# Optimization experiments

Hardware: AMD Instinct MI355X
Metric: run time of the kernel (lower is better)

The kernel has to match this reference:

```python
import jax, jax.numpy as jnp
import numpy as np

N = 100000
E = 3200000
IN_F = 256
OUT_F = 256
CLAMP = 10.0


def setup_inputs() -> dict:
    key = jax.random.key(0)
    k1, k2, k3, k4, k5 = jax.random.split(key, 5)
    x = jax.random.normal(k1, (N, IN_F), dtype=jnp.float32)
    adj_rows = jnp.sort(jax.random.randint(k2, (E,), 0, N, dtype=jnp.int32))
    adj_cols = jax.random.randint(k3, (E,), 0, N, dtype=jnp.int32)
    adj_vals = jax.random.uniform(k4, (E,), dtype=jnp.float32)
    # glorot-ish init (scaled by 0.1 as in the module)
    stdv = 0.1 * np.sqrt(6.0 / (IN_F + OUT_F))
    weight = jax.random.uniform(k5, (IN_F, OUT_F), dtype=jnp.float32,
                                minval=-stdv, maxval=stdv)
    bias = jnp.zeros((OUT_F,), dtype=jnp.float32)
    return {"x": x, "adj_rows": adj_rows, "adj_cols": adj_cols,
            "adj_vals": adj_vals, "weight": weight, "bias": bias}


def reference(x, adj_rows, adj_cols, adj_vals, weight, bias):
    # clamp input
    x = jnp.clip(x, -CLAMP, CLAMP)
    # dense projection: [N, in] @ [in, out]
    support = jnp.clip(x @ weight, -CLAMP, CLAMP)
    # sparse adjacency SpMM: out[r] += val * support[c] for each edge (r, c)
    msgs = adj_vals[:, None] * support[adj_cols]          # [E, out]
    output = jax.ops.segment_sum(msgs, adj_rows, num_segments=N)
    output = jnp.clip(output, -CLAMP, CLAMP)
    output = output + bias
    output = jax.nn.relu(output)
    return jnp.clip(output, -CLAMP, CLAMP)
```

## Files before the change

kernel.cpp:

```cpp
#include <hip/hip_runtime.h>

#define N_NODES 100000
#define N_EDGES 3200000
#define IN_F    256
#define OUT_F   256
#define CLAMP_V 10.0f

typedef __attribute__((ext_vector_type(8))) short bf16x8;
typedef __attribute__((ext_vector_type(4))) float f32x4;

__device__ __forceinline__ float clampf(float v) {
    return fminf(fmaxf(v, -CLAMP_V), CLAMP_V);
}
__device__ __forceinline__ unsigned f2bf(float f) {
    unsigned u = __float_as_uint(f);
    u += 0x7fffu + ((u >> 16) & 1u);
    return u >> 16;
}
__device__ __forceinline__ unsigned cvt_pk_bf16(float lo, float hi) {
    unsigned r;
    asm("v_cvt_pk_bf16_f32 %0, %1, %2" : "=v"(r) : "v"(lo), "v"(hi));
    return r;
}
__device__ __forceinline__ float bflo(unsigned w) { return __uint_as_float(w << 16); }
__device__ __forceinline__ float bfhi(unsigned w) { return __uint_as_float(w & 0xffff0000u); }

__global__ __launch_bounds__(256) void convert_w(
    const float* __restrict__ w, unsigned short* __restrict__ wt) {
    int i = blockIdx.x * 256 + threadIdx.x;
    int k = i & 255, n = i >> 8;
    float v = w[(size_t)k * OUT_F + n];
    int dst = n * 256 + (((k >> 3) ^ (n & 7)) << 3) + (k & 7);
    wt[dst] = (unsigned short)f2bf(v);
}

__global__ __launch_bounds__(256) void build_row_ptr(
    const int* __restrict__ rows, int* __restrict__ row_ptr) {
    int r = blockIdx.x * blockDim.x + threadIdx.x;
    if (r > N_NODES) return;
    int lo = 0, hi = N_EDGES;
    while (lo < hi) {
        int mid = (lo + hi) >> 1;
        if (rows[mid] < r) lo = mid + 1; else hi = mid;
    }
    row_ptr[r] = lo;
}

__global__ __launch_bounds__(1024) void gemm_mfma(
    const float* __restrict__ x, const unsigned short* __restrict__ wt,
    unsigned* __restrict__ sup8, float* __restrict__ scales) {
    __shared__ uint4 wlds[8192];

    const int t    = threadIdx.x;
    const int lane = t & 63;
    const int w    = t >> 6;
    const int wr   = w >> 2;
    const int wc   = w & 3;
    const int l15  = lane & 15;
    const int l4   = lane >> 4;
    const int blockRow = blockIdx.x * 256;

    {
        const uint4* g = (const uint4*)wt;
        #pragma unroll
        for (int i = 0; i < 8; ++i)
            wlds[i * 1024 + t] = g[i * 1024 + t];
    }

    const float* aptr[4];
    #pragma unroll
    for (int m = 0; m < 4; ++m) {
        int r = blockRow + wr * 64 + m * 16 + l15;
        aptr[m] = x + (size_t)(r < N_NODES ? r : N_NODES - 1) * IN_F + l4 * 8;
    }

    f32x4 acc[4][4];
    #pragma unroll
    for (int m = 0; m < 4; ++m)
        #pragma unroll
        for (int n = 0; n < 4; ++n)
            acc[m][n] = (f32x4)0.f;

    __syncthreads();

    #pragma unroll
    for (int s = 0; s < 8; ++s) {
        bf16x8 a[4], b[4];
        #pragma unroll
        for (int m = 0; m < 4; ++m) {
            float4 u0 = *(const float4*)(aptr[m] + s * 32);
            float4 u1 = *(const float4*)(aptr[m] + s * 32 + 4);
            union { unsigned u[4]; bf16x8 v; } pk;
            pk.u[0] = cvt_pk_bf16(clampf(u0.x), clampf(u0.y));
            pk.u[1] = cvt_pk_bf16(clampf(u0.z), clampf(u0.w));
            pk.u[2] = cvt_pk_bf16(clampf(u1.x), clampf(u1.y));
            pk.u[3] = cvt_pk_bf16(clampf(u1.z), clampf(u1.w));
            a[m] = pk.v;
        }
        #pragma unroll
        for (int n = 0; n < 4; ++n) {
            int ncol  = wc * 64 + n * 16 + l15;
            int chunk = ncol * 32 + ((s * 4 + l4) ^ (ncol & 7));
            b[n] = *(const bf16x8*)&wlds[chunk];
        }
        #pragma unroll
        for (int m = 0; m < 4; ++m)
            #pragma unroll
            for (int n = 0; n < 4; ++n)
                acc[m][n] = __builtin_amdgcn_mfma_f32_16x16x32_bf16(
                    a[m], b[n], acc[m][n], 0, 0, 0);
    }

    __syncthreads();
    {
        char* sl = (char*)wlds;
        #pragma unroll
        for (int m = 0; m < 4; ++m) {
            #pragma unroll
            for (int n = 0; n < 4; ++n) {
                int col2 = (wc * 64 + n * 16 + l15) * 2;
                #pragma unroll
                for (int r = 0; r < 4; ++r) {
                    int row = wr * 64 + m * 16 + l4 * 4 + r;
                    int off = row * 512 + (col2 ^ (((row >> 2) & 3) << 4));
                    *(unsigned short*)(sl + off) = (unsigned short)f2bf(clampf(acc[m][n][r]));
                }
            }
        }
    }
    __syncthreads();

    {
        const uint4* sl4 = (const uint4*)wlds;
        const int row = t >> 2;
        const int qt  = t & 3;
        const int swz = (row >> 2) & 3;

        uint4 c[8];
        float mx = 0.f;
        #pragma unroll
        for (int j = 0; j < 8; ++j) {
            c[j] = sl4[row * 32 + ((qt * 8 + j) ^ swz)];
            const unsigned* cu = (const unsigned*)&c[j];
            #pragma unroll
            for (int q = 0; q < 4; ++q)
                mx = fmaxf(mx, fmaxf(fabsf(bflo(cu[q])), fabsf(bfhi(cu[q]))));
        }
        mx = fmaxf(mx, __shfl_xor(mx, 1));
        mx = fmaxf(mx, __shfl_xor(mx, 2));

        const float inv = 127.f / fmaxf(mx, 1e-30f);
        const int grow = blockRow + row;
        if (grow < N_NODES) {
            unsigned p[16];
            #pragma unroll
            for (int j = 0; j < 8; ++j) {
                const unsigned* cu = (const unsigned*)&c[j];
                #pragma unroll
                for (int q = 0; q < 2; ++q) {
                    unsigned b0 = (unsigned)(int)rintf(bflo(cu[q*2+0]) * inv) + 128u;
                    unsigned b1 = (unsigned)(int)rintf(bfhi(cu[q*2+0]) * inv) + 128u;
                    unsigned b2 = (unsigned)(int)rintf(bflo(cu[q*2+1]) * inv) + 128u;
                    unsigned b3 = (unsigned)(int)rintf(bfhi(cu[q*2+1]) * inv) + 128u;
                    p[j*2+q] = b0 | (b1 << 8) | (b2 << 16) | (b3 << 24);
                }
            }
            uint4* dst = (uint4*)(sup8 + (size_t)grow * 64 + qt * 16);
            #pragma unroll
            for (int j = 0; j < 4; ++j)
                dst[j] = *(const uint4*)&p[j * 4];
            if (qt == 0) scales[grow] = mx * (1.f / 127.f);
        }
    }
}

#define FMAQ(g, vs)                                                       \
    S += (vs);                                                            \
    acc[0] += (vs) * (float)((g).x & 0xffu);                              \
    acc[1] += (vs) * (float)(((g).x >> 8) & 0xffu);                       \
    acc[2] += (vs) * (float)(((g).x >> 16) & 0xffu);                      \
    acc[3] += (vs) * (float)((g).x >> 24);                                \
    acc[4] += (vs) * (float)((g).y & 0xffu);                              \
    acc[5] += (vs) * (float)(((g).y >> 8) & 0xffu);                       \
    acc[6] += (vs) * (float)(((g).y >> 16) & 0xffu);                      \
    acc[7] += (vs) * (float)((g).y >> 24);

__global__ __launch_bounds__(256) void spmm_out(
    const unsigned* __restrict__ sup8, const float* __restrict__ scales,
    const int* __restrict__ row_ptr, const int* __restrict__ cols,
    const float* __restrict__ vals, const float* __restrict__ bias,
    float* __restrict__ out) {
    const int wid  = threadIdx.x >> 6;
    const int lane = threadIdx.x & 63;
    const int row  = blockIdx.x * 4 + wid;
    if (row >= N_NODES) return;

    const int e0   = row_ptr[row];
    const int e1   = row_ptr[row + 1];
    const int half = lane >> 5;
    const int c32  = lane & 31;

    const uint2* sup2 = (const uint2*)sup8;
    float acc[8] = {0.f,0.f,0.f,0.f,0.f,0.f,0.f,0.f};
    float S = 0.f;

    int e = e0;
    for (; e + 8 <= e1; e += 8) {
        int   ea = e + half, eb = ea + 2, ec = ea + 4, ed = ea + 6;
        int   ca = cols[ea], cb = cols[eb], cc = cols[ec], cd = cols[ed];
        float va = vals[ea], vb = vals[eb], vc = vals[ec], vd = vals[ed];
        float vsa = va * scales[ca], vsb = vb * scales[cb];
        float vsc = vc * scales[cc], vsd = vd * scales[cd];
        uint2 ga = sup2[(size_t)ca * 32 + c32];
        uint2 gb = sup2[(size_t)cb * 32 + c32];
        uint2 gc = sup2[(size_t)cc * 32 + c32];
        uint2 gd = sup2[(size_t)cd * 32 + c32];
        FMAQ(ga, vsa); FMAQ(gb, vsb); FMAQ(gc, vsc); FMAQ(gd, vsd);
    }
    for (; e + 4 <= e1; e += 4) {
        int   ea = e + half, eb = ea + 2;
        int   ca = cols[ea], cb = cols[eb];
        float va = vals[ea], vb = vals[eb];
        float vsa = va * scales[ca], vsb = vb * scales[cb];
        uint2 ga = sup2[(size_t)ca * 32 + c32];
        uint2 gb = sup2[(size_t)cb * 32 + c32];
        FMAQ(ga, vsa); FMAQ(gb, vsb);
    }
    for (; e < e1; e += 2) {
        int   ea = e + half;
        bool  ok = ea < e1;
        int   ca = cols[ok ? ea : e];
        float va = ok ? vals[ea] : 0.f;
        float vsa = va * scales[ca];
        uint2 ga = sup2[(size_t)ca * 32 + c32];
        FMAQ(ga, vsa);
    }

    S *= 128.f;
    #pragma unroll
    for (int j = 0; j < 8; ++j)
        acc[j] -= S;

    #pragma unroll
    for (int j = 0; j < 8; ++j)
        acc[j] += __shfl_xor(acc[j], 32);

    const float4 b4 = ((const float4*)bias)[c32 * 2 + half];
    f32x4 o;
    o.x = fminf(fmaxf(clampf(acc[half * 4 + 0]) + b4.x, 0.f), CLAMP_V);
    o.y = fminf(fmaxf(clampf(acc[half * 4 + 1]) + b4.y, 0.f), CLAMP_V);
    o.z = fminf(fmaxf(clampf(acc[half * 4 + 2]) + b4.z, 0.f), CLAMP_V);
    o.w = fminf(fmaxf(clampf(acc[half * 4 + 3]) + b4.w, 0.f), CLAMP_V);
    __builtin_nontemporal_store(o, (f32x4*)(out + (size_t)row * OUT_F + c32 * 8 + half * 4));
}

extern "C" void kernel_launch(void* const* d_in, const int* in_sizes, int n_in,
                              void* d_out, int out_size, void* d_ws, size_t ws_size,
                              hipStream_t stream) {
    const float* x        = (const float*)d_in[0];
    const int*   adj_rows = (const int*)d_in[1];
    const int*   adj_cols = (const int*)d_in[2];
    const float* adj_vals = (const float*)d_in[3];
    const float* weight   = (const float*)d_in[4];
    const float* bias     = (const float*)d_in[5];
    float*       out      = (float*)d_out;

    char* ws = (char*)d_ws;
    unsigned*       sup8    = (unsigned*)ws;
    float*          scales  = (float*)(ws + 25600000);
    int*            row_ptr = (int*)(ws + 26000000);
    unsigned short* wt      = (unsigned short*)(ws + 26400064);

    convert_w<<<256, 256, 0, stream>>>(weight, wt);
    build_row_ptr<<<(N_NODES + 1 + 255) / 256, 256, 0, stream>>>(adj_rows, row_ptr);
    gemm_mfma<<<(N_NODES + 255) / 256, 1024, 0, stream>>>(x, wt, sup8, scales);
    spmm_out<<<(N_NODES + 3) / 4, 256, 0, stream>>>(sup8, scales, row_ptr,
                                                    adj_cols, adj_vals, bias, out);
}
```

Measured before the change: 212.4 us.

## Shrink GEMM blocks to 64 rows and read weights directly from global/L2

The GEMM kernel drops from 1024-thread blocks over 256 rows to 256-thread blocks over 64 rows. It stops staging the full 128KB bf16 weight matrix in LDS and instead loads B fragments straight from global memory, using a new k-chunk-major weight layout so each fragment read is contiguous. The aim is to remove the per-block 128KB LDS fill and barrier, raise occupancy with a 32KB LDS footprint, and start MFMA work sooner. In exchange, every block re-reads the weights through L2, and there are four times as many blocks doing so.

```diff
diff --git a/kernel.cpp b/kernel.cpp
--- a/kernel.cpp
+++ b/kernel.cpp
@@ -30,7 +30,7 @@
     int i = blockIdx.x * 256 + threadIdx.x;
     int k = i & 255, n = i >> 8;
     float v = w[(size_t)k * OUT_F + n];
-    int dst = n * 256 + (((k >> 3) ^ (n & 7)) << 3) + (k & 7);
+    int dst = ((k >> 3) << 11) + (n << 3) + (k & 7);
     wt[dst] = (unsigned short)f2bf(v);
 }
 
@@ -46,33 +46,25 @@
     row_ptr[r] = lo;
 }
 
-__global__ __launch_bounds__(1024) void gemm_mfma(
+__global__ __launch_bounds__(256) void gemm_mfma(
     const float* __restrict__ x, const unsigned short* __restrict__ wt,
     unsigned* __restrict__ sup8, float* __restrict__ scales) {
-    __shared__ uint4 wlds[8192];
+    __shared__ char sl[32768];
 
     const int t    = threadIdx.x;
     const int lane = t & 63;
-    const int w    = t >> 6;
-    const int wr   = w >> 2;
-    const int wc   = w & 3;
+    const int wc   = t >> 6;
     const int l15  = lane & 15;
     const int l4   = lane >> 4;
-    const int blockRow = blockIdx.x * 256;
-
-    {
-        const uint4* g = (const uint4*)wt;
-        #pragma unroll
-        for (int i = 0; i < 8; ++i)
-            wlds[i * 1024 + t] = g[i * 1024 + t];
-    }
+    const int blockRow = blockIdx.x * 64;
 
     const float* aptr[4];
     #pragma unroll
     for (int m = 0; m < 4; ++m) {
-        int r = blockRow + wr * 64 + m * 16 + l15;
+        int r = blockRow + m * 16 + l15;
         aptr[m] = x + (size_t)(r < N_NODES ? r : N_NODES - 1) * IN_F + l4 * 8;
     }
+    const unsigned short* bptr = wt + (l4 << 11) + ((wc * 64 + l15) << 3);
 
     f32x4 acc[4][4];
     #pragma unroll
@@ -80,8 +72,6 @@
         #pragma unroll
         for (int n = 0; n < 4; ++n)
             acc[m][n] = (f32x4)0.f;
-
-    __syncthreads();
 
     #pragma unroll
     for (int s = 0; s < 8; ++s) {
@@ -98,11 +88,8 @@
             a[m] = pk.v;
         }
         #pragma unroll
-        for (int n = 0; n < 4; ++n) {
-            int ncol  = wc * 64 + n * 16 + l15;
-            int chunk = ncol * 32 + ((s * 4 + l4) ^ (ncol & 7));
-            b[n] = *(const bf16x8*)&wlds[chunk];
-        }
+        for (int n = 0; n < 4; ++n)
+            b[n] = *(const bf16x8*)(bptr + (s << 13) + (n << 7));
         #pragma unroll
         for (int m = 0; m < 4; ++m)
             #pragma unroll
@@ -111,27 +98,23 @@
                     a[m], b[n], acc[m][n], 0, 0, 0);
     }
 
+    #pragma unroll
+    for (int m = 0; m < 4; ++m) {
+        #pragma unroll
+        for (int n = 0; n < 4; ++n) {
+            int col2 = (wc * 64 + n * 16 + l15) * 2;
+            #pragma unroll
+            for (int r = 0; r < 4; ++r) {
+                int row = m * 16 + l4 * 4 + r;
+                int off = row * 512 + (col2 ^ (((row >> 2) & 3) << 4));
+                *(unsigned short*)(sl + off) = (unsigned short)f2bf(clampf(acc[m][n][r]));
+            }
+        }
+    }
     __syncthreads();
+
     {
-        char* sl = (char*)wlds;
-        #pragma unroll
-        for (int m = 0; m < 4; ++m) {
-            #pragma unroll
-            for (int n = 0; n < 4; ++n) {
-                int col2 = (wc * 64 + n * 16 + l15) * 2;
-                #pragma unroll
-                for (int r = 0; r < 4; ++r) {
-                    int row = wr * 64 + m * 16 + l4 * 4 + r;
-                    int off = row * 512 + (col2 ^ (((row >> 2) & 3) << 4));
-                    *(unsigned short*)(sl + off) = (unsigned short)f2bf(clampf(acc[m][n][r]));
-                }
-            }
-        }
-    }
-    __syncthreads();
-
-    {
-        const uint4* sl4 = (const uint4*)wlds;
+        const uint4* sl4 = (const uint4*)sl;
         const int row = t >> 2;
         const int qt  = t & 3;
         const int swz = (row >> 2) & 3;
@@ -273,7 +256,7 @@
 
     convert_w<<<256, 256, 0, stream>>>(weight, wt);
     build_row_ptr<<<(N_NODES + 1 + 255) / 256, 256, 0, stream>>>(adj_rows, row_ptr);
-    gemm_mfma<<<(N_NODES + 255) / 256, 1024, 0, stream>>>(x, wt, sup8, scales);
+    gemm_mfma<<<(N_NODES + 63) / 64, 256, 0, stream>>>(x, wt, sup8, scales);
     spmm_out<<<(N_NODES + 3) / 4, 256, 0, stream>>>(sup8, scales, row_ptr,
                                                     adj_cols, adj_vals, bias, out);
 }
```

Measured after the change: 200.3 us. 5.7% less time.
